# Optimization experiments

Hardware: AMD Instinct MI355X
Metric: run time of the kernel (lower is better)

The kernel has to match this reference:

```python
import jax, jax.numpy as jnp
import numpy as np

VERTS = [5023, 1256, 314, 79, 20]
SPIRAL_LEN = 9
T_FRAMES = 32
LATENT = 64


def _spiral_conv(x, idx, W, b):
    # x: [B, N, C]; idx: [N, L]; gather spiral neighborhoods then linear
    B = x.shape[0]
    g = x[:, idx.reshape(-1), :].reshape(B, idx.shape[0], -1)  # [B, N, L*C]
    return g @ W.T + b


def _pool(x, rows, cols, vals, n_out):
    # sparse matmul: out[b, rows] += x[b, cols] * vals  (index_select + scatter_add)
    gathered = x[:, cols, :] * vals[None, :, None]
    return jnp.zeros((x.shape[0], n_out, x.shape[2]), x.dtype).at[:, rows, :].add(gathered)


def _lstm_dir(x, Wih, Whh, bih, bhh, reverse):
    # x: [T, B, D]; PyTorch gate order i, f, g, o
    Bz, H = x.shape[1], Whh.shape[1]
    bias = bih + bhh
    def step(carry, xt):
        h, c = carry
        g = xt @ Wih.T + h @ Whh.T + bias
        i, f, gg, o = jnp.split(g, 4, axis=-1)
        c = jax.nn.sigmoid(f) * c + jax.nn.sigmoid(i) * jnp.tanh(gg)
        h = jax.nn.sigmoid(o) * jnp.tanh(c)
        return (h, c), h
    init = (jnp.zeros((Bz, H), x.dtype), jnp.zeros((Bz, H), x.dtype))
    _, hs = jax.lax.scan(step, init, x, reverse=reverse)
    return hs


def _forward(audio_hidden, vertices, actor,
             sp_idx0, sp_idx1, sp_idx2, sp_idx3,
             d0_rows, d0_cols, d0_vals, d1_rows, d1_cols, d1_vals,
             d2_rows, d2_cols, d2_vals, d3_rows, d3_cols, d3_vals,
             u0_rows, u0_cols, u0_vals, u1_rows, u1_cols, u1_vals,
             u2_rows, u2_cols, u2_vals, u3_rows, u3_cols, u3_vals,
             enc_W0, enc_b0, enc_W1, enc_b1, enc_W2, enc_b2, enc_W3, enc_b3,
             enc_lin_W, enc_lin_b, dec_lin_W, dec_lin_b,
             dec_W0, dec_b0, dec_W1, dec_b1, dec_W2, dec_b2, dec_W3, dec_b3,
             dec_W4, dec_b4, aud_W, aud_b,
             l0_Wih, l0_Whh, l0_bih, l0_bhh, l12_Wih, l12_Whh, l12_bih, l12_bhh):
    ah = audio_hidden
    if ah.shape[1] % 2 != 0:
        ah = ah[:, :ah.shape[1] - 1]
    tv = vertices.shape[1]
    if ah.shape[1] > 2 * tv:
        ah = ah[:, :2 * tv]
    elif ah.shape[1] < 2 * tv:
        tv = ah.shape[1] // 2
    hs = ah.reshape(1, ah.shape[1] // 2, ah.shape[2] * 2)[:, :tv]  # [1, T, 1536]
    audio_emb = hs @ aud_W.T + aud_b                                # [1, T, LATENT]
    # --- mesh encoder on actor template: (spiral conv -> ELU -> down pool) x4 -> Linear ---
    sp = (sp_idx0, sp_idx1, sp_idx2, sp_idx3)
    down = ((d0_rows, d0_cols, d0_vals), (d1_rows, d1_cols, d1_vals),
            (d2_rows, d2_cols, d2_vals), (d3_rows, d3_cols, d3_vals))
    encp = ((enc_W0, enc_b0), (enc_W1, enc_b1), (enc_W2, enc_b2), (enc_W3, enc_b3))
    x = actor
    for i in range(4):
        x = jax.nn.elu(_spiral_conv(x, sp[i], *encp[i]))
        x = _pool(x, *down[i], VERTS[i + 1])
    z = x.reshape(x.shape[0], -1) @ enc_lin_W.T + enc_lin_b        # [1, LATENT]
    actor_emb = jnp.broadcast_to(z[:, None, :], audio_emb.shape)
    # --- 3-layer bidirectional LSTM ---
    h = jnp.concatenate([audio_emb, actor_emb], axis=-1).transpose(1, 0, 2)  # [T, 1, 2*LATENT]
    for layer in range(3):
        if layer == 0:
            Wih, Whh, bih, bhh = l0_Wih, l0_Whh, l0_bih, l0_bhh
        else:
            Wih, Whh, bih, bhh = l12_Wih[layer - 1], l12_Whh[layer - 1], l12_bih[layer - 1], l12_bhh[layer - 1]
        f = _lstm_dir(h, Wih[0], Whh[0], bih[0], bhh[0], False)
        r = _lstm_dir(h, Wih[1], Whh[1], bih[1], bhh[1], True)
        h = jnp.concatenate([f, r], axis=-1)
    latent = h.transpose(1, 0, 2)[0]                               # [T, LATENT]
    # --- mesh decoder, batched over all frames (replaces the python per-frame loop) ---
    up = ((u0_rows, u0_cols, u0_vals), (u1_rows, u1_cols, u1_vals),
          (u2_rows, u2_cols, u2_vals), (u3_rows, u3_cols, u3_vals))
    decp = ((dec_W0, dec_b0), (dec_W1, dec_b1), (dec_W2, dec_b2), (dec_W3, dec_b3))
    y = latent @ dec_lin_W.T + dec_lin_b                           # [T, 20*256]
    y = y.reshape(y.shape[0], VERTS[4], -1)                        # [T, 20, 256]
    for i in range(4):
        j = 3 - i
        y = _pool(y, *up[j], VERTS[j])
        y = jax.nn.elu(_spiral_conv(y, sp[j], *decp[i]))
    y = _spiral_conv(y, sp[0], dec_W4, dec_b4)                     # [T, 5023, 3]
    return y + actor                                               # broadcast residual, == vstacked preds


def setup_inputs() -> dict:
    key = jax.random.key(0)
    ks = iter(jax.random.split(key, 96))
    def nrm(shape, s=0.05):
        return jax.random.normal(next(ks), shape, jnp.float32) * s
    def rint(shape, hi):
        return jax.random.randint(next(ks), shape, 0, hi)
    inp = {}
    inp['audio_hidden'] = nrm((1, 2 * T_FRAMES, 768), 1.0)
    inp['vertices'] = nrm((1, T_FRAMES, VERTS[0], 3), 1.0)
    inp['actor'] = nrm((1, VERTS[0], 3), 1.0)
    for i in range(4):
        inp['sp_idx%d' % i] = rint((VERTS[i], SPIRAL_LEN), VERTS[i])
    for i in range(4):
        nnz = 3 * VERTS[i + 1]
        inp['d%d_rows' % i] = rint((nnz,), VERTS[i + 1])
        inp['d%d_cols' % i] = rint((nnz,), VERTS[i])
        inp['d%d_vals' % i] = jax.random.uniform(next(ks), (nnz,), jnp.float32)
    for i in range(4):
        nnz = 3 * VERTS[i]
        inp['u%d_rows' % i] = rint((nnz,), VERTS[i])
        inp['u%d_cols' % i] = rint((nnz,), VERTS[i + 1])
        inp['u%d_vals' % i] = jax.random.uniform(next(ks), (nnz,), jnp.float32)
    OC = [32, 64, 128, 256]
    ic = 3
    for i in range(4):
        inp['enc_W%d' % i] = nrm((OC[i], ic * SPIRAL_LEN))
        inp['enc_b%d' % i] = nrm((OC[i],))
        ic = OC[i]
    inp['enc_lin_W'] = nrm((LATENT, VERTS[4] * OC[3]))
    inp['enc_lin_b'] = nrm((LATENT,))
    inp['dec_lin_W'] = nrm((VERTS[4] * OC[3], LATENT))
    inp['dec_lin_b'] = nrm((VERTS[4] * OC[3],))
    dic = [256, 256, 128, 64]
    doc = [256, 128, 64, 32]
    for i in range(4):
        inp['dec_W%d' % i] = nrm((doc[i], dic[i] * SPIRAL_LEN))
        inp['dec_b%d' % i] = nrm((doc[i],))
    inp['dec_W4'] = nrm((3, OC[0] * SPIRAL_LEN))
    inp['dec_b4'] = nrm((3,))
    inp['aud_W'] = nrm((LATENT, 1536))
    inp['aud_b'] = nrm((LATENT,))
    H = LATENT // 2
    inp['l0_Wih'] = nrm((2, 4 * H, 2 * LATENT))
    inp['l0_Whh'] = nrm((2, 4 * H, H))
    inp['l0_bih'] = nrm((2, 4 * H))
    inp['l0_bhh'] = nrm((2, 4 * H))
    inp['l12_Wih'] = nrm((2, 2, 4 * H, 2 * H))
    inp['l12_Whh'] = nrm((2, 2, 4 * H, H))
    inp['l12_bih'] = nrm((2, 2, 4 * H))
    inp['l12_bhh'] = nrm((2, 2, 4 * H))
    return inp


def reference(audio_hidden, vertices, actor,
              sp_idx0, sp_idx1, sp_idx2, sp_idx3,
              d0_rows, d0_cols, d0_vals, d1_rows, d1_cols, d1_vals,
              d2_rows, d2_cols, d2_vals, d3_rows, d3_cols, d3_vals,
              u0_rows, u0_cols, u0_vals, u1_rows, u1_cols, u1_vals,
              u2_rows, u2_cols, u2_vals, u3_rows, u3_cols, u3_vals,
              enc_W0, enc_b0, enc_W1, enc_b1, enc_W2, enc_b2, enc_W3, enc_b3,
              enc_lin_W, enc_lin_b, dec_lin_W, dec_lin_b,
              dec_W0, dec_b0, dec_W1, dec_b1, dec_W2, dec_b2, dec_W3, dec_b3,
              dec_W4, dec_b4, aud_W, aud_b,
              l0_Wih, l0_Whh, l0_bih, l0_bhh, l12_Wih, l12_Whh, l12_bih, l12_bhh):
    return _forward(audio_hidden, vertices, actor,
                    sp_idx0, sp_idx1, sp_idx2, sp_idx3,
                    d0_rows, d0_cols, d0_vals, d1_rows, d1_cols, d1_vals,
                    d2_rows, d2_cols, d2_vals, d3_rows, d3_cols, d3_vals,
                    u0_rows, u0_cols, u0_vals, u1_rows, u1_cols, u1_vals,
                    u2_rows, u2_cols, u2_vals, u3_rows, u3_cols, u3_vals,
                    enc_W0, enc_b0, enc_W1, enc_b1, enc_W2, enc_b2, enc_W3, enc_b3,
                    enc_lin_W, enc_lin_b, dec_lin_W, dec_lin_b,
                    dec_W0, dec_b0, dec_W1, dec_b1, dec_W2, dec_b2, dec_W3, dec_b3,
                    dec_W4, dec_b4, aud_W, aud_b,
                    l0_Wih, l0_Whh, l0_bih, l0_bhh, l12_Wih, l12_Whh, l12_bih, l12_bhh)
```

## Files before the change

### kernel.cpp

```cpp
#include <hip/hip_runtime.h>
#include <cstdint>
#include <cstddef>


typedef unsigned short u16;
typedef __attribute__((ext_vector_type(8))) short short8;
typedef __attribute__((ext_vector_type(4))) float float4v;
#define CDIV(a,b) (((a)+(b)-1)/(b))
#define POOL_CAP 64

__device__ __forceinline__ float bf(u16 u){ return __uint_as_float(((unsigned)u)<<16); }
__device__ __forceinline__ u16 fb(float x){
  unsigned u = __float_as_uint(x);
  unsigned r = u + 0x7fffu + ((u>>16)&1u);
  return (u16)(r>>16);
}
__device__ __forceinline__ float lo16(unsigned u){ return __uint_as_float(u<<16); }
__device__ __forceinline__ float hi16(unsigned u){ return __uint_as_float(u & 0xffff0000u); }

struct WCast { const float* src[7]; int cum[8]; };
struct Lists {
  const int* rows[8];
  int nnz[8];
  int curoff[8];
  int lstoff[8];
};

__global__ void __launch_bounds__(256) setup_k(
    Lists L, int totN, int NF, int* __restrict__ curBase, int* __restrict__ lstBase,
    WCast C, int totW, int NC, u16* __restrict__ Wbf,
    const float* __restrict__ audio, const float* __restrict__ audW,
    const float* __restrict__ audB, float* __restrict__ h0,
    const float* __restrict__ actor, const int* __restrict__ sp0,
    const float* __restrict__ encW0, const float* __restrict__ encB0,
    u16* __restrict__ outA){
  int blk = blockIdx.x;
  int tid = threadIdx.x;
  if (blk < NF){
    int i = blk*256 + tid;
    if (i < totN){
      int off = i, k = 0;
      while (off >= L.nnz[k]){ off -= L.nnz[k]; k++; }
      int r = L.rows[k][off];
      int p = atomicAdd(curBase + L.curoff[k] + r, 1);
      if (p < POOL_CAP) lstBase[L.lstoff[k] + r*POOL_CAP + p] = off;
    }
    return;
  }
  blk -= NF;
  if (blk < NC){
    int i = blk*256 + tid;
    if (i < totW){
      int k = 0;
      while (i >= C.cum[k+1]) k++;
      Wbf[i] = fb(C.src[k][i - C.cum[k]]);
    }
    return;
  }
  blk -= NC;
  if (blk < 32){
    int t = blk;
    int f = tid >> 2, sl = tid & 3;
    const float4* x4 = (const float4*)(audio + t*1536);
    const float4* w4 = (const float4*)(audW + f*1536);
    float acc = 0.f;
    for (int k=sl; k<384; k+=4){
      float4 xv = x4[k], wv = w4[k];
      acc += xv.x*wv.x + xv.y*wv.y + xv.z*wv.z + xv.w*wv.w;
    }
    acc += __shfl_down(acc, 2, 64);
    acc += __shfl_down(acc, 1, 64);
    if (sl == 0) h0[t*128 + f] = acc + audB[f];
    return;
  }
  blk -= 32;
  int i = blk*256 + tid;
  if (i >= 5023*32) return;
  int o = i % 32; int v = i / 32;
  const float* wrow = encW0 + (size_t)o*27;
  const int* vix = sp0 + v*9;
  float acc = encB0[o];
  for (int s=0;s<9;s++){
    const float* xr = actor + (size_t)vix[s]*3;
    acc += xr[0]*wrow[s*3] + xr[1]*wrow[s*3+1] + xr[2]*wrow[s*3+2];
  }
  if (acc < 0.f) acc = expm1f(acc);
  outA[i] = fb(acc);
}

template<int IC, int BN, int BM>
__global__ void __launch_bounds__(256) conv_mfma(
    const u16* __restrict__ x, const int* __restrict__ idx,
    const u16* __restrict__ Wb, const float* __restrict__ bias,
    u16* __restrict__ out, int V, int OC, int M){
  constexpr int K = 9*IC;
  constexpr int KC = K/32;
  constexpr int NT = BN/16;
  constexpr int MT = BM/64;
  constexpr int LOG2 = (IC==32?5: IC==64?6: IC==128?7:8);
  constexpr int AST = 40;
  __shared__ u16 Asm[2][BM*AST];
  __shared__ u16 Bsm[2][BN*AST];
  __shared__ int rowB[BM], rowV[BM];
  __shared__ int sidx[BM*9];
  int t = threadIdx.x;
  int m0 = blockIdx.x*BM;
  int o0 = blockIdx.y*BN;
  if (t < BM){
    int mg = m0 + t;
    if (mg < M){ int b = mg / V; rowB[t] = b; rowV[t] = mg - b*V; }
    else rowB[t] = -1;
  }
  __syncthreads();
  for (int i=t; i<BM*9; i+=256){
    int r = i/9, s = i - r*9;
    sidx[i] = (rowB[r] >= 0) ? idx[rowV[r]*9 + s] : 0;
  }
  int lane = t & 63, wave = t >> 6;
  int quad = lane >> 4, col = lane & 15;
  float4v acc[MT][NT];
  #pragma unroll
  for (int mi=0;mi<MT;mi++)
    #pragma unroll
    for (int nt=0;nt<NT;nt++) acc[mi][nt] = (float4v)0.f;

  uint4 aval[MT]; uint4 bval;
  auto fetch = [&](int kc){
    int s  = (kc*32) >> LOG2;
    int c0 = (kc*32) & (IC-1);
    #pragma unroll
    for (int rpt=0; rpt<MT; ++rpt){
      int seg = t + 256*rpt;
      int arow = seg >> 2, aq = seg & 3;
      int b = rowB[arow];
      uint4 v = {0u,0u,0u,0u};
      if (b >= 0){
        int ix = sidx[arow*9 + s];
        v = *(const uint4*)(x + ((size_t)b*V + ix)*IC + c0 + aq*8);
      }
      aval[rpt] = v;
    }
    if (t < BN*4){
      int br = t >> 2, bq = t & 3;
      bval = *(const uint4*)(Wb + (size_t)(o0+br)*K + kc*32 + bq*8);
    }
  };

  __syncthreads();
  fetch(0);

  for (int kc = 0; kc < KC; ++kc){
    int buf = kc & 1;
    #pragma unroll
    for (int rpt=0; rpt<MT; ++rpt){
      int seg = t + 256*rpt;
      int arow = seg >> 2, aq = seg & 3;
      *(uint4*)&Asm[buf][arow*AST + aq*8] = aval[rpt];
    }
    if (t < BN*4){
      int br = t >> 2, bq = t & 3;
      *(uint4*)&Bsm[buf][br*AST + bq*8] = bval;
    }
    __syncthreads();
    if (kc+1 < KC) fetch(kc+1);
    short8 a[MT];
    #pragma unroll
    for (int mi=0;mi<MT;mi++)
      a[mi] = *(const short8*)&Asm[buf][(wave*MT*16 + mi*16 + col)*AST + quad*8];
    #pragma unroll
    for (int nt=0; nt<NT; ++nt){
      short8 bfr = *(const short8*)&Bsm[buf][(nt*16 + col)*AST + quad*8];
      #pragma unroll
      for (int mi=0;mi<MT;mi++)
        acc[mi][nt] = __builtin_amdgcn_mfma_f32_16x16x32_bf16(a[mi], bfr, acc[mi][nt], 0, 0, 0);
    }
  }
  #pragma unroll
  for (int mi=0;mi<MT;mi++){
    #pragma unroll
    for (int nt=0; nt<NT; ++nt){
      int o = o0 + nt*16 + col;
      float bv = bias[o];
      #pragma unroll
      for (int r=0;r<4;r++){
        int mg = m0 + wave*MT*16 + mi*16 + quad*4 + r;
        if (mg < M){
          float val = acc[mi][nt][r] + bv;
          if (val < 0.f) val = expm1f(val);
          out[(size_t)mg*OC + o] = fb(val);
        }
      }
    }
  }
}

__global__ void pool_g8_k(const u16* __restrict__ x, const int* __restrict__ cols,
                          const float* __restrict__ vals, const int* __restrict__ cur,
                          const int* __restrict__ lst, u16* __restrict__ out,
                          int B, int Vin, int Vout, int C){
  int C8 = C >> 3;
  int total = B*Vout*C8;
  int i = blockIdx.x*blockDim.x + threadIdx.x;
  if (i >= total) return;
  int c8 = i % C8; int tt = i / C8; int r = tt % Vout; int b = tt / Vout;
  int deg = cur[r]; if (deg > POOL_CAP) deg = POOL_CAP;
  const int* le = lst + r*POOL_CAP;
  float a0=0.f,a1=0.f,a2=0.f,a3=0.f,a4=0.f,a5=0.f,a6=0.f,a7=0.f;
  for (int k=0;k<deg;k++){
    int e = le[k];
    float v = vals[e];
    uint4 xv = *(const uint4*)(x + ((size_t)b*Vin + (size_t)cols[e])*C + c8*8);
    a0 += v*lo16(xv.x); a1 += v*hi16(xv.x);
    a2 += v*lo16(xv.y); a3 += v*hi16(xv.y);
    a4 += v*lo16(xv.z); a5 += v*hi16(xv.z);
    a6 += v*lo16(xv.w); a7 += v*hi16(xv.w);
  }
  uint4 o;
  o.x = ((unsigned)fb(a0)) | (((unsigned)fb(a1))<<16);
  o.y = ((unsigned)fb(a2)) | (((unsigned)fb(a3))<<16);
  o.z = ((unsigned)fb(a4)) | (((unsigned)fb(a5))<<16);
  o.w = ((unsigned)fb(a6)) | (((unsigned)fb(a7))<<16);
  *(uint4*)(out + ((size_t)b*Vout + (size_t)r)*C + c8*8) = o;
}

__global__ void __launch_bounds__(256) enc_lin_k(
    const u16* __restrict__ x, const float* __restrict__ W,
    const float* __restrict__ b, float* __restrict__ h0){
  int f = blockIdx.x;
  int t = threadIdx.x;
  const ushort4* x4 = (const ushort4*)x;
  const float4* w4 = (const float4*)(W + (size_t)f*5120);
  float acc = 0.f;
  for (int k=t; k<1280; k+=256){
    ushort4 xv = x4[k]; float4 wv = w4[k];
    acc += bf(xv.x)*wv.x + bf(xv.y)*wv.y + bf(xv.z)*wv.z + bf(xv.w)*wv.w;
  }
  #pragma unroll
  for (int off=32; off; off>>=1) acc += __shfl_down(acc, off, 64);
  __shared__ float red[4];
  if ((t & 63) == 0) red[t>>6] = acc;
  __syncthreads();
  if (t < 32){
    float zf = b[f] + red[0] + red[1] + red[2] + red[3];
    h0[t*128 + 64 + f] = zf;
  }
}

__device__ __forceinline__ float sigm(float x){ return 1.f/(1.f+__expf(-x)); }
__device__ __forceinline__ float tanhfast(float x){ return 1.f - 2.f/(__expf(2.f*x)+1.f); }

__global__ void __launch_bounds__(256) lstm3_k(
    const float* __restrict__ h0,
    const float* __restrict__ l0_Wih, const float* __restrict__ l0_Whh,
    const float* __restrict__ l0_bih, const float* __restrict__ l0_bhh,
    const float* __restrict__ l12_Wih, const float* __restrict__ l12_Whh,
    const float* __restrict__ l12_bih, const float* __restrict__ l12_bhh,
    float* __restrict__ latent){
  __shared__ __align__(16) u16 xb[32*136];
  __shared__ __align__(16) float xp[2*32*128];
  __shared__ __align__(16) u16 obuf[32*64];
  __shared__ __align__(16) u16 hsh[2][32];
  __shared__ float bias_l[256];
  int t = threadIdx.x;
  int lane = t & 63, wave = t >> 6;
  int quad = lane >> 4, col = lane & 15;
  int dir = t >> 7;
  bool rev = (dir == 1);
  int w2 = (t >> 6) & 1;
  int unit = w2*16 + col;
  int jj = quad*32 + unit;

  for (int i=t;i<32*128;i+=256){ int tt=i>>7, k=i&127; xb[tt*136+k]=fb(h0[i]); }

  for (int layer=0; layer<3; layer++){
    int IN = (layer==0)?128:64;
    const float *Wih,*Whh,*bih,*bhh;
    if (layer==0){ Wih=l0_Wih; Whh=l0_Whh; bih=l0_bih; bhh=l0_bhh; }
    else {
      int mb=(layer-1)*2;
      Wih=l12_Wih + (size_t)mb*128*64; Whh=l12_Whh + (size_t)mb*128*32;
      bih=l12_bih + mb*128; bhh=l12_bhh + mb*128;
    }
    const float* WhhD = Whh + (size_t)dir*128*32 + (size_t)jj*32;
    unsigned whh[16];
    #pragma unroll
    for (int k=0;k<16;k++){
      float2 w = *(const float2*)&WhhD[2*k];
      whh[k] = ((unsigned)fb(w.x)) | (((unsigned)fb(w.y))<<16);
    }
    bias_l[t] = bih[dir*128 + (t&127)] + bhh[dir*128 + (t&127)];
    if (quad == 0) hsh[dir][unit] = 0;
    float creg = 0.f;
    __syncthreads();

    {
      int dirA = wave >> 1, o0 = (wave & 1)*64;
      const float* WA = Wih + (size_t)dirA*128*IN;
      float4v acc[2][4];
      #pragma unroll
      for (int mi=0;mi<2;mi++)
        #pragma unroll
        for (int nt=0;nt<4;nt++) acc[mi][nt] = (float4v)0.f;
      for (int kc=0; kc<IN/32; ++kc){
        short8 bfrag[4];
        #pragma unroll
        for (int nt=0;nt<4;nt++){
          const float* src = WA + (size_t)(o0+nt*16+col)*IN + kc*32 + quad*8;
          float4 w0 = *(const float4*)src;
          float4 w1 = *(const float4*)(src+4);
          alignas(16) u16 tmp[8] = {fb(w0.x),fb(w0.y),fb(w0.z),fb(w0.w),
                                    fb(w1.x),fb(w1.y),fb(w1.z),fb(w1.w)};
          bfrag[nt] = *(const short8*)tmp;
        }
        short8 afrag[2];
        #pragma unroll
        for (int mi=0;mi<2;mi++)
          afrag[mi] = *(const short8*)&xb[(mi*16+col)*136 + kc*32 + quad*8];
        #pragma unroll
        for (int nt=0;nt<4;nt++)
          #pragma unroll
          for (int mi=0;mi<2;mi++)
            acc[mi][nt] = __builtin_amdgcn_mfma_f32_16x16x32_bf16(afrag[mi], bfrag[nt], acc[mi][nt], 0, 0, 0);
      }
      #pragma unroll
      for (int mi=0;mi<2;mi++)
        #pragma unroll
        for (int nt=0;nt<4;nt++){
          int j = o0 + nt*16 + col;
          float bv = bias_l[dirA*128 + j];
          #pragma unroll
          for (int r=0;r<4;r++){
            int tt = mi*16 + quad*4 + r;
            xp[dirA*4096 + tt*128 + j] = acc[mi][nt][r] + bv;
          }
        }
    }
    __syncthreads();

    for (int s=0;s<32;s++){
      int tx = rev ? (31-s) : s;
      float g = xp[dir*4096 + tx*128 + jj];
      const uint4* h4 = (const uint4*)hsh[dir];
      float a0=0.f,a1=0.f,a2=0.f,a3=0.f;
      #pragma unroll
      for (int k=0;k<4;k++){
        uint4 hv = h4[k];
        unsigned u0=whh[4*k], u1=whh[4*k+1], u2=whh[4*k+2], u3=whh[4*k+3];
        a0 = fmaf(lo16(hv.x), lo16(u0), a0);
        a0 = fmaf(hi16(hv.x), hi16(u0), a0);
        a1 = fmaf(lo16(hv.y), lo16(u1), a1);
        a1 = fmaf(hi16(hv.y), hi16(u1), a1);
        a2 = fmaf(lo16(hv.z), lo16(u2), a2);
        a2 = fmaf(hi16(hv.z), hi16(u2), a2);
        a3 = fmaf(lo16(hv.w), lo16(u3), a3);
        a3 = fmaf(hi16(hv.w), hi16(u3), a3);
      }
      g += (a0+a1) + (a2+a3);
      float act = (quad == 2) ? tanhfast(g) : sigm(g);
      float gi = __shfl(act, col, 64);
      float gf = __shfl(act, 16+col, 64);
      float gg = __shfl(act, 32+col, 64);
      float go = __shfl(act, 48+col, 64);
      if (quad == 0){
        float cn = gf*creg + gi*gg;
        float hn = go*tanhfast(cn);
        creg = cn;
        u16 hb = fb(hn);
        hsh[dir][unit] = hb;
        obuf[tx*64 + dir*32 + unit] = hb;
      }
      __syncthreads();
    }
    if (layer < 2){
      for (int i=t;i<32*64;i+=256){ int tt=i>>6, k=i&63; xb[tt*136+k]=obuf[i]; }
      __syncthreads();
    }
  }
  for (int i=t;i<32*64;i+=256) latent[i] = bf(obuf[i]);
}

__global__ void dec_lin_k(const float* __restrict__ latent, const float* __restrict__ W,
                          const float* __restrict__ b, u16* __restrict__ y){
  int i = blockIdx.x*blockDim.x + threadIdx.x;
  if (i >= 32*5120) return;
  int r = i % 5120, t = i / 5120;
  const float4* x4 = (const float4*)(latent + t*64);
  const float4* w4 = (const float4*)(W + (size_t)r*64);
  float acc = b[r];
  #pragma unroll
  for (int k=0;k<16;k++){
    float4 xv=x4[k]; float4 wv=w4[k];
    acc += xv.x*wv.x+xv.y*wv.y+xv.z*wv.z+xv.w*wv.w;
  }
  y[i] = fb(acc);
}

__global__ void final_k(const u16* __restrict__ x, const int* __restrict__ idx,
                        const float* __restrict__ W, const float* __restrict__ bias,
                        const float* __restrict__ actor, float* __restrict__ out){
  __shared__ float Wsm[3*288];
  __shared__ float bsm[3];
  int t = threadIdx.x;
  for (int i=t;i<864;i+=256) Wsm[i]=W[i];
  if (t<3) bsm[t]=bias[t];
  __syncthreads();
  int g = blockIdx.x*256 + t;
  if (g >= 32*5023) return;
  int v = g % 5023, b = g / 5023;
  const u16* xb = x + (size_t)b*5023*32;
  const int* vix = idx + v*9;
  float a0=bsm[0], a1=bsm[1], a2=bsm[2];
  for (int s=0;s<9;s++){
    const ushort4* xr = (const ushort4*)(xb + (size_t)vix[s]*32);
    #pragma unroll
    for (int k=0;k<8;k++){
      ushort4 xv = xr[k];
      float x0=bf(xv.x), x1=bf(xv.y), x2=bf(xv.z), x3=bf(xv.w);
      int kk = s*32 + k*4;
      a0 += x0*Wsm[kk] + x1*Wsm[kk+1] + x2*Wsm[kk+2] + x3*Wsm[kk+3];
      a1 += x0*Wsm[288+kk] + x1*Wsm[288+kk+1] + x2*Wsm[288+kk+2] + x3*Wsm[288+kk+3];
      a2 += x0*Wsm[576+kk] + x1*Wsm[576+kk+1] + x2*Wsm[576+kk+2] + x3*Wsm[576+kk+3];
    }
  }
  out[(size_t)g*3+0] = a0 + actor[v*3+0];
  out[(size_t)g*3+1] = a1 + actor[v*3+1];
  out[(size_t)g*3+2] = a2 + actor[v*3+2];
}

extern "C" void kernel_launch(void* const* d_in, const int* in_sizes, int n_in,
                              void* d_out, int out_size, void* d_ws, size_t ws_size,
                              hipStream_t stream){
  (void)in_sizes; (void)n_in; (void)out_size; (void)ws_size;

  const float* audio = (const float*)d_in[0];
  const float* actor = (const float*)d_in[2];
  const int* sp[4]   = {(const int*)d_in[3],(const int*)d_in[4],(const int*)d_in[5],(const int*)d_in[6]};
  const int* drows[4]; const int* dcols[4]; const float* dvals[4];
  for (int i=0;i<4;i++){ drows[i]=(const int*)d_in[7+3*i]; dcols[i]=(const int*)d_in[8+3*i]; dvals[i]=(const float*)d_in[9+3*i]; }
  const int* urows[4]; const int* ucols[4]; const float* uvals[4];
  for (int i=0;i<4;i++){ urows[i]=(const int*)d_in[19+3*i]; ucols[i]=(const int*)d_in[20+3*i]; uvals[i]=(const float*)d_in[21+3*i]; }
  const float* encW[4]={(const float*)d_in[31],(const float*)d_in[33],(const float*)d_in[35],(const float*)d_in[37]};
  const float* encB[4]={(const float*)d_in[32],(const float*)d_in[34],(const float*)d_in[36],(const float*)d_in[38]};
  const float* enc_lin_W=(const float*)d_in[39]; const float* enc_lin_b=(const float*)d_in[40];
  const float* dec_lin_W=(const float*)d_in[41]; const float* dec_lin_b=(const float*)d_in[42];
  const float* decW[5]={(const float*)d_in[43],(const float*)d_in[45],(const float*)d_in[47],(const float*)d_in[49],(const float*)d_in[51]};
  const float* decB[5]={(const float*)d_in[44],(const float*)d_in[46],(const float*)d_in[48],(const float*)d_in[50],(const float*)d_in[52]};
  const float* audW=(const float*)d_in[53]; const float* audB=(const float*)d_in[54];
  const float* l0_Wih=(const float*)d_in[55]; const float* l0_Whh=(const float*)d_in[56];
  const float* l0_bih=(const float*)d_in[57]; const float* l0_bhh=(const float*)d_in[58];
  const float* l12_Wih=(const float*)d_in[59]; const float* l12_Whh=(const float*)d_in[60];
  const float* l12_bih=(const float*)d_in[61]; const float* l12_bhh=(const float*)d_in[62];
  float* out = (float*)d_out;

  char* base = (char*)d_ws;
  u16* A  = (u16*)base;
  u16* Bb = (u16*)(base + 10287104);
  int* curBase = (int*)(base + 30891520);
  int* lstBase = (int*)(base + 30924928);
  u16* Wbf = (u16*)(base + 33060224);
  float* sm = (float*)(base + 35788160);
  float* h0     = sm;
  float* latent = sm + 4096;

  const int wsz[7] = {64*288, 128*576, 256*1152, 256*2304, 128*2304, 64*1152, 32*576};
  WCast WC; int wcum = 0;
  const float* wsrc[7] = {encW[1],encW[2],encW[3],decW[0],decW[1],decW[2],decW[3]};
  int wo[7];
  for (int k=0;k<7;k++){ WC.src[k]=wsrc[k]; WC.cum[k]=wcum; wo[k]=wcum; wcum+=wsz[k]; }
  WC.cum[7]=wcum;

  const int pVout[8] = {1256,314,79,20,5023,1256,314,79};
  const int pNnz[8]  = {3768,942,237,60,15069,3768,942,237};
  Lists L; int curoff=0, lstoff=0, totnnz=0;
  const int* prow[8] = {drows[0],drows[1],drows[2],drows[3],urows[0],urows[1],urows[2],urows[3]};
  int curo[8], lsto[8];
  for (int k=0;k<8;k++){
    L.rows[k]=prow[k]; L.nnz[k]=pNnz[k];
    L.curoff[k]=curoff; L.lstoff[k]=lstoff;
    curo[k]=curoff; lsto[k]=lstoff;
    curoff += pVout[k]; lstoff += pVout[k]*POOL_CAP; totnnz += pNnz[k];
  }
  hipMemsetAsync(curBase, 0, (size_t)curoff*4, stream);

  int NF = CDIV(totnnz,256), NC = CDIV(wcum,256), NC3 = CDIV(5023*32,256);
  setup_k<<<NF+NC+32+NC3,256,0,stream>>>(L, totnnz, NF, curBase, lstBase,
                                         WC, wcum, NC, Wbf,
                                         audio, audW, audB, h0,
                                         actor, sp[0], encW[0], encB[0], A);

  pool_g8_k<<<CDIV(1256*4,256),256,0,stream>>>(A, dcols[0], dvals[0], curBase+curo[0], lstBase+lsto[0], Bb, 1, 5023, 1256, 32);
  conv_mfma<32,64,64><<<dim3(CDIV(1256,64),1),256,0,stream>>>(Bb, sp[1], Wbf+wo[0], encB[1], A, 1256, 64, 1256);
  pool_g8_k<<<CDIV(314*8,256),256,0,stream>>>(A, dcols[1], dvals[1], curBase+curo[1], lstBase+lsto[1], Bb, 1, 1256, 314, 64);
  conv_mfma<64,64,64><<<dim3(CDIV(314,64),2),256,0,stream>>>(Bb, sp[2], Wbf+wo[1], encB[2], A, 314, 128, 314);
  pool_g8_k<<<CDIV(79*16,256),256,0,stream>>>(A, dcols[2], dvals[2], curBase+curo[2], lstBase+lsto[2], Bb, 1, 314, 79, 128);
  conv_mfma<128,64,64><<<dim3(CDIV(79,64),4),256,0,stream>>>(Bb, sp[3], Wbf+wo[2], encB[3], A, 79, 256, 79);
  pool_g8_k<<<CDIV(20*32,256),256,0,stream>>>(A, dcols[3], dvals[3], curBase+curo[3], lstBase+lsto[3], Bb, 1, 79, 20, 256);

  enc_lin_k<<<64,256,0,stream>>>(Bb, enc_lin_W, enc_lin_b, h0);

  lstm3_k<<<1,256,0,stream>>>(h0, l0_Wih, l0_Whh, l0_bih, l0_bhh,
                              l12_Wih, l12_Whh, l12_bih, l12_bhh, latent);

  dec_lin_k<<<CDIV(32*5120,256),256,0,stream>>>(latent, dec_lin_W, dec_lin_b, A);

  pool_g8_k<<<CDIV(32*79*32,256),256,0,stream>>>(A, ucols[3], uvals[3], curBase+curo[7], lstBase+lsto[7], Bb, 32, 20, 79, 256);
  conv_mfma<256,64,64><<<dim3(CDIV(2528,64),4),256,0,stream>>>(Bb, sp[3], Wbf+wo[3], decB[0], A, 79, 256, 2528);

  pool_g8_k<<<CDIV(32*314*32,256),256,0,stream>>>(A, ucols[2], uvals[2], curBase+curo[6], lstBase+lsto[6], Bb, 32, 79, 314, 256);
  conv_mfma<256,64,64><<<dim3(CDIV(10048,64),2),256,0,stream>>>(Bb, sp[2], Wbf+wo[4], decB[1], A, 314, 128, 10048);

  pool_g8_k<<<CDIV(32*1256*16,256),256,0,stream>>>(A, ucols[1], uvals[1], curBase+curo[5], lstBase+lsto[5], Bb, 32, 314, 1256, 128);
  conv_mfma<128,64,128><<<dim3(CDIV(40192,128),1),256,0,stream>>>(Bb, sp[1], Wbf+wo[5], decB[2], A, 1256, 64, 40192);

  pool_g8_k<<<CDIV(32*5023*8,256),256,0,stream>>>(A, ucols[0], uvals[0], curBase+curo[4], lstBase+lsto[4], Bb, 32, 1256, 5023, 64);
  conv_mfma<64,32,128><<<dim3(CDIV(160736,128),1),256,0,stream>>>(Bb, sp[0], Wbf+wo[6], decB[3], A, 5023, 32, 160736);

  final_k<<<CDIV(32*5023,256),256,0,stream>>>(A, sp[0], decW[4], decB[4], actor, out);
}
```

Baseline: 574.0 us.

## Run each LSTM direction's recurrence in a single wave without block barriers

The recurrent part of the LSTM previously used all four waves with a block-wide __syncthreads after every timestep. Now one wave per direction runs the whole recurrence, each lane computing two gates with fp32 Whh weights held in registers. Gates are exchanged with a single xor shuffle, and the per-step barrier is removed because communication through shared memory stays within a wave. The next timestep's input projection is prefetched, and the hidden state is kept in fp32. The cost is doubled per-lane FMA work and higher register pressure from 64 weight registers, and the code relies on wave-synchronous ordering of the shared-memory hidden state.

After: 569.2 us. Within noise of the previous version (-0.8%).

```diff
diff --git a/kernel.cpp b/kernel.cpp
--- a/kernel.cpp
+++ b/kernel.cpp
@@ -259,16 +259,11 @@
   __shared__ __align__(16) u16 xb[32*136];
   __shared__ __align__(16) float xp[2*32*128];
   __shared__ __align__(16) u16 obuf[32*64];
-  __shared__ __align__(16) u16 hsh[2][32];
+  __shared__ __align__(16) float hsh32[2][32];
   __shared__ float bias_l[256];
   int t = threadIdx.x;
   int lane = t & 63, wave = t >> 6;
   int quad = lane >> 4, col = lane & 15;
-  int dir = t >> 7;
-  bool rev = (dir == 1);
-  int w2 = (t >> 6) & 1;
-  int unit = w2*16 + col;
-  int jj = quad*32 + unit;
 
   for (int i=t;i<32*128;i+=256){ int tt=i>>7, k=i&127; xb[tt*136+k]=fb(h0[i]); }
 
@@ -281,16 +276,7 @@
       Wih=l12_Wih + (size_t)mb*128*64; Whh=l12_Whh + (size_t)mb*128*32;
       bih=l12_bih + mb*128; bhh=l12_bhh + mb*128;
     }
-    const float* WhhD = Whh + (size_t)dir*128*32 + (size_t)jj*32;
-    unsigned whh[16];
-    #pragma unroll
-    for (int k=0;k<16;k++){
-      float2 w = *(const float2*)&WhhD[2*k];
-      whh[k] = ((unsigned)fb(w.x)) | (((unsigned)fb(w.y))<<16);
-    }
-    bias_l[t] = bih[dir*128 + (t&127)] + bhh[dir*128 + (t&127)];
-    if (quad == 0) hsh[dir][unit] = 0;
-    float creg = 0.f;
+    bias_l[t] = bih[(t>>7)*128 + (t&127)] + bhh[(t>>7)*128 + (t&127)];
     __syncthreads();
 
     {
@@ -337,40 +323,60 @@
     }
     __syncthreads();
 
-    for (int s=0;s<32;s++){
-      int tx = rev ? (31-s) : s;
-      float g = xp[dir*4096 + tx*128 + jj];
-      const uint4* h4 = (const uint4*)hsh[dir];
-      float a0=0.f,a1=0.f,a2=0.f,a3=0.f;
+    if (wave < 2){
+      int dir = wave; bool rev = (dir == 1);
+      int unit = lane & 31, gh = lane >> 5;
+      int jA = gh*32 + unit;
+      int jB = (gh+2)*32 + unit;
+      const float* WD = Whh + (size_t)dir*128*32;
+      float wA[32], wB[32];
       #pragma unroll
-      for (int k=0;k<4;k++){
-        uint4 hv = h4[k];
-        unsigned u0=whh[4*k], u1=whh[4*k+1], u2=whh[4*k+2], u3=whh[4*k+3];
-        a0 = fmaf(lo16(hv.x), lo16(u0), a0);
-        a0 = fmaf(hi16(hv.x), hi16(u0), a0);
-        a1 = fmaf(lo16(hv.y), lo16(u1), a1);
-        a1 = fmaf(hi16(hv.y), hi16(u1), a1);
-        a2 = fmaf(lo16(hv.z), lo16(u2), a2);
-        a2 = fmaf(hi16(hv.z), hi16(u2), a2);
-        a3 = fmaf(lo16(hv.w), lo16(u3), a3);
-        a3 = fmaf(hi16(hv.w), hi16(u3), a3);
+      for (int k=0;k<32;k++){ wA[k]=WD[(size_t)jA*32+k]; wB[k]=WD[(size_t)jB*32+k]; }
+      float* hsd = &hsh32[dir][0];
+      if (gh==0) hsd[unit] = 0.f;
+      float creg = 0.f;
+      const float* xpd = xp + dir*4096;
+      float gAc = xpd[(rev?31:0)*128 + jA];
+      float gBc = xpd[(rev?31:0)*128 + jB];
+      #pragma unroll 1
+      for (int s=0;s<32;s++){
+        int tx = rev ? (31-s) : s;
+        int sn = (s+1 < 32) ? s+1 : 31;
+        int txn = rev ? (31-sn) : sn;
+        float gA2 = xpd[txn*128 + jA];
+        float gB2 = xpd[txn*128 + jB];
+        const float4* h4 = (const float4*)hsd;
+        float a0=0.f,a1=0.f,a2=0.f,a3=0.f,b0=0.f,b1=0.f,b2=0.f,b3=0.f;
+        #pragma unroll
+        for (int k=0;k<8;k++){
+          float4 hv = h4[k];
+          a0=fmaf(hv.x,wA[4*k+0],a0); b0=fmaf(hv.x,wB[4*k+0],b0);
+          a1=fmaf(hv.y,wA[4*k+1],a1); b1=fmaf(hv.y,wB[4*k+1],b1);
+          a2=fmaf(hv.z,wA[4*k+2],a2); b2=fmaf(hv.z,wB[4*k+2],b2);
+          a3=fmaf(hv.w,wA[4*k+3],a3); b3=fmaf(hv.w,wB[4*k+3],b3);
+        }
+        float gA = gAc + ((a0+a1)+(a2+a3));
+        float gB = gBc + ((b0+b1)+(b2+b3));
+        float actA = sigm(gA);
+        float tB = sigm(gh ? gB : 2.f*gB);
+        float actB = gh ? tB : (2.f*tB - 1.f);
+        float pA = __shfl_xor(actA, 32, 64);
+        float pB = __shfl_xor(actB, 32, 64);
+        float gi = gh ? pA : actA;
+        float gf = gh ? actA : pA;
+        float gg = gh ? pB : actB;
+        float go = gh ? actB : pB;
+        float cn = fmaf(gf, creg, gi*gg);
+        float hn = go * tanhfast(cn);
+        creg = cn;
+        if (gh==0){
+          hsd[unit] = hn;
+          obuf[tx*64 + dir*32 + unit] = fb(hn);
+        }
+        gAc = gA2; gBc = gB2;
       }
-      g += (a0+a1) + (a2+a3);
-      float act = (quad == 2) ? tanhfast(g) : sigm(g);
-      float gi = __shfl(act, col, 64);
-      float gf = __shfl(act, 16+col, 64);
-      float gg = __shfl(act, 32+col, 64);
-      float go = __shfl(act, 48+col, 64);
-      if (quad == 0){
-        float cn = gf*creg + gi*gg;
-        float hn = go*tanhfast(cn);
-        creg = cn;
-        u16 hb = fb(hn);
-        hsh[dir][unit] = hb;
-        obuf[tx*64 + dir*32 + unit] = hb;
-      }
-      __syncthreads();
-    }
+    }
+    __syncthreads();
     if (layer < 2){
       for (int i=t;i<32*64;i+=256){ int tt=i>>6, k=i&63; xb[tt*136+k]=obuf[i]; }
       __syncthreads();
```
